# Kernel tuning notes

Hardware: AMD Instinct MI355X
Metric: run time of the kernel (lower is better)

## Reference

```python
import jax, jax.numpy as jnp
import numpy as np

NATTRS, NOBJS = 250, 400
N = NATTRS + NOBJS           # 650 graph nodes
E = 100000                   # edges
D_IN, D_HID, D_NODE = 512, 4096, 512
FEAT, EMB, B = 2048, 800, 256
LN_EPS = 1e-5


def setup_inputs() -> dict:
    key = jax.random.key(0)
    ks = jax.random.split(key, 32)
    w = lambda k, shape: (jax.random.normal(k, shape, jnp.float32) / np.sqrt(shape[-1])).astype(jnp.float32)
    return {
        'img': jax.random.normal(ks[0], (B, FEAT), jnp.float32),
        'nodes': jax.random.normal(ks[1], (N, D_IN), jnp.float32),
        'edge_src': jax.random.randint(ks[2], (E,), 0, N),
        'edge_dst': jax.random.randint(ks[3], (E,), 0, N),
        'W1l': w(ks[4], (D_HID, D_IN)), 'b1': jnp.zeros((D_HID,), jnp.float32), 'W1r': w(ks[5], (D_HID, D_IN)),
        'W2l': w(ks[6], (D_NODE, D_HID)), 'b2': jnp.zeros((D_NODE,), jnp.float32), 'W2r': w(ks[7], (D_NODE, D_HID)),
        'Wp1': w(ks[8], (1200, 2 * D_NODE)), 'bp1': jnp.zeros((1200,), jnp.float32),
        'Wp2': w(ks[9], (EMB, 1200)), 'bp2': jnp.zeros((EMB,), jnp.float32),
        'gp': jnp.ones((EMB,), jnp.float32), 'bpn': jnp.zeros((EMB,), jnp.float32),
        'Wi1': w(ks[10], (768, FEAT)), 'bi1': jnp.zeros((768,), jnp.float32),
        'Wi2': w(ks[11], (1000, 768)), 'bi2': jnp.zeros((1000,), jnp.float32),
        'Wi3': w(ks[12], (EMB, 1000)), 'bi3': jnp.zeros((EMB,), jnp.float32),
        'gi': jnp.ones((EMB,), jnp.float32), 'bin_': jnp.zeros((EMB,), jnp.float32),
    }


def _segment_mean(x, src, dst, n):
    # gather source features, mean-aggregate at destinations (PyG SAGEConv 'mean')
    agg = jax.ops.segment_sum(x[src], dst, num_segments=n)
    deg = jax.ops.segment_sum(jnp.ones_like(dst, dtype=x.dtype), dst, num_segments=n)
    return agg / jnp.clip(deg, 1.0)[:, None]


def _sage(x, src, dst, Wl, bl, Wr):
    # out_i = lin_l(mean_{j in N(i)} x_j) + lin_r(x_i); lin_r has no bias in PyG
    return _segment_mean(x, src, dst, x.shape[0]) @ Wl.T + bl + x @ Wr.T


def _ln(x, g, b):
    m = x.mean(-1, keepdims=True)
    v = ((x - m) ** 2).mean(-1, keepdims=True)
    return (x - m) / jnp.sqrt(v + LN_EPS) * g + b


def reference(img, nodes, edge_src, edge_dst, W1l, b1, W1r, W2l, b2, W2r,
              Wp1, bp1, Wp2, bp2, gp, bpn, Wi1, bi1, Wi2, bi2, Wi3, bi3, gi, bin_):
    # GCN backbone (dropout is identity in eval)
    h = jax.nn.relu(_sage(nodes, edge_src, edge_dst, W1l, b1, W1r))
    out_nodes = _sage(h, edge_src, edge_dst, W2l, b2, W2r)          # [N, 512]
    # all attr-obj pairs: attr repeated per obj, objs tiled per attr
    attr = out_nodes[:NATTRS]
    obj = out_nodes[NATTRS:]
    pa = jnp.repeat(attr, NOBJS, axis=0)                            # [P, 512]
    po = jnp.tile(obj, (NATTRS, 1))                                 # [P, 512]
    pairs = jnp.concatenate([pa, po], axis=1)                       # [P, 1024]
    # pair_fc: Linear-ReLU -> Linear -> LayerNorm
    p = jax.nn.relu(pairs @ Wp1.T + bp1)
    p = _ln(p @ Wp2.T + bp2, gp, bpn)                               # [P, 800]
    # img_fc: two hidden Linear-ReLU -> Linear -> LayerNorm
    i = jax.nn.relu(img @ Wi1.T + bi1)
    i = jax.nn.relu(i @ Wi2.T + bi2)
    i = _ln(i @ Wi3.T + bi3, gi, bin_)                              # [B, 800]
    return i @ p.T                                                  # [B, P]
```

## Files before the change

kernel.cpp:

```cpp
#include <hip/hip_runtime.h>

#define NN 650
#define NE 100000

typedef short bf16x8_t __attribute__((ext_vector_type(8)));
typedef short s16x4_t __attribute__((ext_vector_type(4)));
typedef float f32x4_t __attribute__((ext_vector_type(4)));

__device__ __forceinline__ unsigned short f2bf(float f) {
  union { float f; unsigned u; } x; x.f = f;
  unsigned r = x.u + 0x7fffu + ((x.u >> 16) & 1u);
  return (unsigned short)(r >> 16);
}
__device__ __forceinline__ float bf2f(unsigned short u) {
  union { unsigned u; float f; } x; x.u = ((unsigned)u) << 16; return x.f;
}

typedef const __attribute__((address_space(1))) unsigned int* gptr_t;
typedef __attribute__((address_space(3))) unsigned int* lptr_t;
__device__ __forceinline__ void gl_lds16(const unsigned short* g, unsigned short* l) {
  __builtin_amdgcn_global_load_lds((gptr_t)g, (lptr_t)l, 16, 0, 0);
}

__global__ void k_scatter(const int* __restrict__ src, const int* __restrict__ dst,
                          float* __restrict__ C, float* __restrict__ deg) {
  int e = blockIdx.x * 256 + threadIdx.x;
  if (e < NE) {
    int s = src[e], d = dst[e];
    atomicAdd(&C[d * NN + s], 1.0f);
    atomicAdd(&deg[d], 1.0f);
  }
}

__global__ void k_adj_norm(const float* __restrict__ C, const float* __restrict__ deg,
                           unsigned short* __restrict__ Cn) {
  int idx = blockIdx.x * 256 + threadIdx.x;
  if (idx >= 768 * 672) return;
  int i = idx / 672, j = idx - i * 672;
  float v = (i < NN && j < NN) ? C[i * NN + j] / fmaxf(deg[i], 1.0f) : 0.0f;
  Cn[idx] = f2bf(v);
}

#define MAXJ 12
struct CvtDesc { const float* src; unsigned short* dst; int Mvalid, Kin, ldi, off, ldo, nElem, nblk; };
struct CvtPack { CvtDesc d[MAXJ]; };
__global__ void k_cvt_all(CvtPack P) {
  int b = blockIdx.x;
  int j = 0;
  while (b >= P.d[j].nblk) { b -= P.d[j].nblk; ++j; }
  const CvtDesc D = P.d[j];
  int idx = b * 256 + threadIdx.x;
  if (idx >= D.nElem) return;
  int r = idx / D.ldo, c = idx - r * D.ldo;
  D.dst[idx] = (r < D.Mvalid && c < D.Kin) ? f2bf(D.src[(size_t)r * D.ldi + D.off + c]) : (unsigned short)0;
}

__global__ void k_ttr(const unsigned short* __restrict__ in, unsigned short* __restrict__ out,
                      int ldi, int ldo) {
  __shared__ unsigned short tile[64][65];
  const int c0 = blockIdx.x * 64, r0 = blockIdx.y * 64;
  const int t = threadIdx.x;
  const int rl = t >> 4, cl = (t & 15) * 4;
#pragma unroll
  for (int rr = 0; rr < 4; ++rr) {
    s16x4_t v = *(const s16x4_t*)(in + (size_t)(r0 + rl + rr * 16) * ldi + c0 + cl);
#pragma unroll
    for (int j = 0; j < 4; ++j) tile[rl + rr * 16][cl + j] = (unsigned short)v[j];
  }
  __syncthreads();
  if (r0 + cl < ldo) {
#pragma unroll
    for (int cc = 0; cc < 4; ++cc) {
      int crow = rl + cc * 16;
      unsigned short o[4] = { tile[cl + 0][crow], tile[cl + 1][crow],
                              tile[cl + 2][crow], tile[cl + 3][crow] };
      *(s16x4_t*)(out + (size_t)(c0 + crow) * ldo + r0 + cl) = *(s16x4_t*)o;
    }
  }
}

__global__ void k_pgen(const float* __restrict__ Pa, const float* __restrict__ Po,
                       unsigned short* __restrict__ P, int r0, int rows) {
  int g = blockIdx.x * 256 + threadIdx.x;
  if (g >= rows * 152) return;
  int lp = g / 152, k = (g - lp * 152) * 8;
  int p = r0 + lp;
  unsigned short t8[8];
  if (p < 100000) {
    int a = p / 400, o = p - a * 400;
    const float* pa = Pa + (size_t)a * 1216 + k;
    const float* po = Po + (size_t)o * 1216 + k;
    float4 x1 = *(const float4*)(pa);
    float4 x2 = *(const float4*)(pa + 4);
    float4 y1 = *(const float4*)(po);
    float4 y2 = *(const float4*)(po + 4);
    t8[0] = f2bf(fmaxf(x1.x + y1.x, 0.f)); t8[1] = f2bf(fmaxf(x1.y + y1.y, 0.f));
    t8[2] = f2bf(fmaxf(x1.z + y1.z, 0.f)); t8[3] = f2bf(fmaxf(x1.w + y1.w, 0.f));
    t8[4] = f2bf(fmaxf(x2.x + y2.x, 0.f)); t8[5] = f2bf(fmaxf(x2.y + y2.y, 0.f));
    t8[6] = f2bf(fmaxf(x2.z + y2.z, 0.f)); t8[7] = f2bf(fmaxf(x2.w + y2.w, 0.f));
  } else {
#pragma unroll
    for (int j = 0; j < 8; ++j) t8[j] = 0;
  }
  *(bf16x8_t*)(P + (size_t)lp * 1216 + k) = *(bf16x8_t*)t8;
}

__global__ void k_stats_fin(float* __restrict__ S, float* __restrict__ SS) {
  int i = blockIdx.x * 256 + threadIdx.x;
  if (i >= 100096) return;
  float s = S[i], ss = SS[i];
  float m = s * (1.0f / 800.0f);
  float var = ss * (1.0f / 800.0f) - m * m;
  S[i] = m;
  SS[i] = rsqrtf(fmaxf(var, 0.f) + 1e-5f);
}

__global__ void k_fin_on(const float* __restrict__ acc, const float* __restrict__ bias,
                         unsigned short* __restrict__ out) {
  int i = blockIdx.x * 256 + threadIdx.x;
  if (i >= 768 * 512) return;
  int r = i >> 9, c = i & 511;
  out[i] = f2bf(r < 650 ? acc[i] + bias[c] : 0.f);
}
__global__ void k_fin_rb(const float* __restrict__ acc, const float* __restrict__ bias,
                         unsigned short* __restrict__ out, int nElem, int cols, int Nv) {
  int i = blockIdx.x * 256 + threadIdx.x;
  if (i >= nElem) return;
  int c = i % cols;
  float v = 0.f;
  if (c < Nv) v = fmaxf(acc[i] + bias[c], 0.f);
  out[i] = f2bf(v);
}

__global__ void k_prep_i(const unsigned short* __restrict__ iB,
                         const float* __restrict__ gp, const float* __restrict__ bpn,
                         unsigned short* __restrict__ iG,
                         float* __restrict__ c1, float* __restrict__ c2) {
  const int row = blockIdx.x, t = threadIdx.x;
  float s1 = 0.f, s2 = 0.f;
  if (t < 100) {
    bf16x8_t v = *(const bf16x8_t*)(iB + (size_t)row * 800 + t * 8);
    unsigned short o[8];
#pragma unroll
    for (int j = 0; j < 8; ++j) {
      float f = bf2f((unsigned short)v[j]);
      float g = gp[t * 8 + j];
      s1 += f * g; s2 += f * bpn[t * 8 + j];
      o[j] = f2bf(f * g);
    }
    *(bf16x8_t*)(iG + (size_t)row * 800 + t * 8) = *(bf16x8_t*)o;
  }
#pragma unroll
  for (int off = 32; off > 0; off >>= 1) { s1 += __shfl_down(s1, off); s2 += __shfl_down(s2, off); }
  __shared__ float sh[4];
  int w = t >> 6, lane = t & 63;
  if (lane == 0) { sh[w] = s1; sh[2 + w] = s2; }
  __syncthreads();
  if (t == 0) { c1[row] = sh[0] + sh[1]; c2[row] = sh[2] + sh[3]; }
}

#define BK 32
template<int OUT_BF, int RELU, int LNF, int QST, int SK>
__launch_bounds__(256)
__global__ void k_gemm128(const unsigned short* __restrict__ A,
                          const unsigned short* __restrict__ B,
                          const float* __restrict__ bias,
                          const float* __restrict__ addb,
                          void* __restrict__ Cout,
                          int K, int ldc,
                          int Mvalid, int Nvalid, int Nstore, int swap, int swz,
                          const float* __restrict__ lnm, const float* __restrict__ lninv,
                          const float* __restrict__ lnc1, const float* __restrict__ lnc2,
                          float* __restrict__ sumP, float* __restrict__ ssP) {
  __shared__ unsigned short As[2][128 * BK];
  __shared__ unsigned short Bs[2][128 * BK];
  const int tid = threadIdx.x;
  const int w = tid >> 6, lane = tid & 63;
  int bx = blockIdx.x, by = blockIdx.y;
  if (swz) {
    int T = gridDim.x * gridDim.y;
    int flat = blockIdx.x + gridDim.x * blockIdx.y;
    int xcd = flat & 7, s = flat >> 3;
    int qq = T >> 3, rr = T & 7;
    int slot = (xcd < rr ? xcd * (qq + 1) : rr * (qq + 1) + (xcd - rr) * qq) + s;
    bx = slot % gridDim.x; by = slot / gridDim.x;
  }
  const int bm = swap ? by : bx;
  const int bn = swap ? bx : by;
  const int m0 = bm * 128, n0 = bn * 128;
  const int wm = w & 1, wn = w >> 1;
  const int lr = lane & 15, q = lane >> 4;

  const int srow = w * 32 + (lane >> 2);
  const int mw_ = ((lane >> 2) & 3) ^ ((lane >> 4) & 3);
  const int scol = (((lane & 3) ^ mw_) * 8);
  const int mr_ = (lane & 3) ^ ((lane >> 2) & 3);
  const int qe = ((q ^ mr_) * 8);

  int nt = K / BK, kt0 = 0;
  if (SK) { int Ksl = K / (int)gridDim.z; nt = Ksl / BK; kt0 = blockIdx.z * (Ksl / BK); }

  const unsigned short* Ag = A + (size_t)(m0 + srow) * K + (size_t)kt0 * BK + scol;
  const unsigned short* Bg = B + (size_t)(n0 + srow) * K + (size_t)kt0 * BK + scol;
  const int so0 = (w * 32) * BK;
  const int so1 = (w * 32 + 16) * BK;

  f32x4_t acc[4][4];
#pragma unroll
  for (int r = 0; r < 4; ++r)
#pragma unroll
    for (int t = 0; t < 4; ++t) { f32x4_t z = {0.f, 0.f, 0.f, 0.f}; acc[r][t] = z; }

  gl_lds16(Ag, &As[0][so0]); gl_lds16(Ag + 16 * (size_t)K, &As[0][so1]);
  gl_lds16(Bg, &Bs[0][so0]); gl_lds16(Bg + 16 * (size_t)K, &Bs[0][so1]);
  Ag += BK; Bg += BK;

  for (int t = 0; t < nt; ++t) {
    const int cur = t & 1;
    __syncthreads();
    if (t + 1 < nt) {
      const int nxt = cur ^ 1;
      gl_lds16(Ag, &As[nxt][so0]); gl_lds16(Ag + 16 * (size_t)K, &As[nxt][so1]);
      gl_lds16(Bg, &Bs[nxt][so0]); gl_lds16(Bg + 16 * (size_t)K, &Bs[nxt][so1]);
      Ag += BK; Bg += BK;
    }
    bf16x8_t af[4], bfv[4];
#pragma unroll
    for (int r = 0; r < 4; ++r)
      af[r] = *(const bf16x8_t*)(&As[cur][(wm * 64 + r * 16 + lr) * BK + qe]);
#pragma unroll
    for (int tt = 0; tt < 4; ++tt)
      bfv[tt] = *(const bf16x8_t*)(&Bs[cur][(wn * 64 + tt * 16 + lr) * BK + qe]);
#pragma unroll
    for (int r = 0; r < 4; ++r)
#pragma unroll
      for (int tt = 0; tt < 4; ++tt)
        acc[r][tt] = __builtin_amdgcn_mfma_f32_16x16x32_bf16(af[r], bfv[tt], acc[r][tt], 0, 0, 0);
  }

  if (SK) {
#pragma unroll
    for (int r = 0; r < 4; ++r)
#pragma unroll
      for (int t = 0; t < 4; ++t)
#pragma unroll
        for (int e = 0; e < 4; ++e) {
          int gm = m0 + wm * 64 + r * 16 + q * 4 + e;
          int gn = n0 + wn * 64 + t * 16 + lr;
          if (gm < Mvalid && gn < Nvalid)
            atomicAdd((float*)Cout + (size_t)gm * ldc + gn, acc[r][t][e]);
        }
  } else if (QST) {
#pragma unroll
    for (int r = 0; r < 4; ++r) {
#pragma unroll
      for (int e = 0; e < 4; ++e) {
        const int gm = m0 + wm * 64 + r * 16 + q * 4 + e;
        float s = 0.f, ss = 0.f;
#pragma unroll
        for (int t = 0; t < 4; ++t) {
          const int gn = n0 + wn * 64 + t * 16 + lr;
          float v = 0.f;
          if (gm < Mvalid && gn < Nvalid) v = acc[r][t][e] + bias[gn];
          if (gn < Nstore)
            ((unsigned short*)Cout)[(size_t)gm * ldc + gn] = f2bf(v);
          s += v; ss += v * v;
        }
#pragma unroll
        for (int m = 1; m < 16; m <<= 1) {
          s += __shfl_xor(s, m);
          ss += __shfl_xor(ss, m);
        }
        if (lr == 0 && gm < Mvalid) {
          atomicAdd(&sumP[gm], s);
          atomicAdd(&ssP[gm], ss);
        }
      }
    }
  } else {
#pragma unroll
    for (int r = 0; r < 4; ++r) {
#pragma unroll
      for (int t = 0; t < 4; ++t) {
#pragma unroll
        for (int e = 0; e < 4; ++e) {
          int gm = m0 + wm * 64 + r * 16 + q * 4 + e;
          int gn = n0 + wn * 64 + t * 16 + lr;
          if (gn < Nstore) {
            float v = 0.f;
            if (gm < Mvalid && gn < Nvalid) {
              v = acc[r][t][e];
              if (LNF) {
                v = lninv[gn] * (v - lnm[gn] * lnc1[gm]) + lnc2[gm];
              } else {
                if (bias) v += bias[gn];
                if (addb) v += addb[(size_t)gm * ldc + gn];
                if (RELU) v = fmaxf(v, 0.f);
              }
            }
            if (OUT_BF) ((unsigned short*)Cout)[(size_t)gm * ldc + gn] = f2bf(v);
            else        ((float*)Cout)[(size_t)gm * ldc + gn] = v;
          }
        }
      }
    }
  }
}

__global__ void k_ln_img(const float* __restrict__ in, const float* __restrict__ bb,
                         unsigned short* __restrict__ out,
                         const float* __restrict__ g, const float* __restrict__ b) {
  const int row = blockIdx.x, t = threadIdx.x;
  float v[4]; float s = 0.f, ss = 0.f; int j = 0;
  for (int idx = t; idx < 800; idx += 256, ++j) {
    float x = in[(size_t)row * 800 + idx] + bb[idx];
    v[j] = x; s += x; ss += x * x;
  }
#pragma unroll
  for (int off = 32; off > 0; off >>= 1) {
    s += __shfl_down(s, off);
    ss += __shfl_down(ss, off);
  }
  __shared__ float sh[8];
  int wave = t >> 6, lane = t & 63;
  if (lane == 0) { sh[wave] = s; sh[4 + wave] = ss; }
  __syncthreads();
  if (t == 0) {
    float S = sh[0] + sh[1] + sh[2] + sh[3];
    float SS = sh[4] + sh[5] + sh[6] + sh[7];
    float m = S * (1.0f / 800.0f);
    float var = SS * (1.0f / 800.0f) - m * m;
    sh[0] = m; sh[1] = rsqrtf(fmaxf(var, 0.f) + 1e-5f);
  }
  __syncthreads();
  float m = sh[0], inv = sh[1];
  j = 0;
  for (int idx = t; idx < 800; idx += 256, ++j) {
    float y = (v[j] - m) * inv * g[idx] + b[idx];
    out[(size_t)row * 800 + idx] = f2bf(y);
  }
}

extern "C" void kernel_launch(void* const* d_in, const int* in_sizes, int n_in,
                              void* d_out, int out_size, void* d_ws, size_t ws_size,
                              hipStream_t stream) {
  (void)in_sizes; (void)n_in; (void)out_size; (void)ws_size;
  const float* img  = (const float*)d_in[0];
  const float* nodes= (const float*)d_in[1];
  const int* esrc   = (const int*)d_in[2];
  const int* edst   = (const int*)d_in[3];
  const float* W1l  = (const float*)d_in[4];
  const float* b1   = (const float*)d_in[5];
  const float* W1r  = (const float*)d_in[6];
  const float* W2l  = (const float*)d_in[7];
  const float* b2   = (const float*)d_in[8];
  const float* W2r  = (const float*)d_in[9];
  const float* Wp1  = (const float*)d_in[10];
  const float* bp1  = (const float*)d_in[11];
  const float* Wp2  = (const float*)d_in[12];
  const float* bp2  = (const float*)d_in[13];
  const float* gp   = (const float*)d_in[14];
  const float* bpn  = (const float*)d_in[15];
  const float* Wi1  = (const float*)d_in[16];
  const float* bi1  = (const float*)d_in[17];
  const float* Wi2  = (const float*)d_in[18];
  const float* bi2  = (const float*)d_in[19];
  const float* Wi3  = (const float*)d_in[20];
  const float* bi3  = (const float*)d_in[21];
  const float* gi   = (const float*)d_in[22];
  const float* binp = (const float*)d_in[23];

  char* wsp = (char*)d_ws;
  auto alloc = [&](size_t bytes) -> void* {
    void* p = (void*)wsp; wsp += (bytes + 255) & ~(size_t)255; return p;
  };
  unsigned short* onB    = (unsigned short*)alloc((size_t)768 * 512 * 2);
  unsigned short* Wp1LB  = (unsigned short*)alloc((size_t)1280 * 512 * 2);
  unsigned short* Wp1RB  = (unsigned short*)alloc((size_t)1280 * 512 * 2);
  unsigned short* Wp2B   = (unsigned short*)alloc((size_t)896 * 1216 * 2);
  float* PaB             = (float*)alloc((size_t)256 * 1216 * 4);
  float* PoB             = (float*)alloc((size_t)512 * 1216 * 4);
  unsigned short* imgB   = (unsigned short*)alloc((size_t)256 * 2048 * 2);
  unsigned short* Wi1B   = (unsigned short*)alloc((size_t)768 * 2048 * 2);
  unsigned short* Wi2B   = (unsigned short*)alloc((size_t)1024 * 768 * 2);
  unsigned short* Wi3B   = (unsigned short*)alloc((size_t)896 * 1024 * 2);
  unsigned short* i1B    = (unsigned short*)alloc((size_t)256 * 768 * 2);
  unsigned short* i2B    = (unsigned short*)alloc((size_t)256 * 1024 * 2);
  float* i3F             = (float*)alloc((size_t)256 * 800 * 4);
  unsigned short* iB     = (unsigned short*)alloc((size_t)256 * 800 * 2);
  unsigned short* iG     = (unsigned short*)alloc((size_t)256 * 800 * 2);
  float* c1B             = (float*)alloc(256 * 4);
  float* c2B             = (float*)alloc(256 * 4);
  float* mArr            = (float*)alloc((size_t)100096 * 4);
  float* ivArr           = (float*)alloc((size_t)100096 * 4);
  unsigned short* qB     = (unsigned short*)alloc((size_t)100096 * 800 * 2);

  char* swp = (char*)qB;
  auto salloc = [&](size_t bytes) -> void* {
    void* p = (void*)swp; swp += (bytes + 255) & ~(size_t)255; return p;
  };
  float* adjC            = (float*)salloc((size_t)NN * NN * 4);
  float* deg             = (float*)salloc(NN * 4);
  unsigned short* Cn     = (unsigned short*)salloc((size_t)768 * 672 * 2);
  unsigned short* nodesB = (unsigned short*)salloc((size_t)768 * 512 * 2);
  unsigned short* nodesT = (unsigned short*)salloc((size_t)512 * 672 * 2);
  unsigned short* agg1   = (unsigned short*)salloc((size_t)768 * 512 * 2);
  float* tmp1            = (float*)salloc((size_t)768 * 4096 * 4);
  unsigned short* hB     = (unsigned short*)salloc((size_t)768 * 4096 * 2);
  unsigned short* hT     = (unsigned short*)salloc((size_t)4096 * 672 * 2);
  unsigned short* agg2   = (unsigned short*)salloc((size_t)768 * 4096 * 2);
  float* tmp2            = (float*)salloc((size_t)768 * 512 * 4);
  unsigned short* W1lB   = (unsigned short*)salloc((size_t)4096 * 512 * 2);
  unsigned short* W1rB   = (unsigned short*)salloc((size_t)4096 * 512 * 2);
  unsigned short* W2lB   = (unsigned short*)salloc((size_t)512 * 4096 * 2);
  unsigned short* W2rB   = (unsigned short*)salloc((size_t)512 * 4096 * 2);
  float* F1              = (float*)salloc((size_t)256 * 768 * 4);
  float* F2              = (float*)salloc((size_t)256 * 1024 * 4);

  unsigned short* Pch = (unsigned short*)d_out;

  hipMemsetAsync(adjC, 0, (size_t)NN * NN * 4, stream);
  hipMemsetAsync(deg, 0, NN * 4, stream);
  hipMemsetAsync(mArr, 0, (size_t)100096 * 4, stream);
  hipMemsetAsync(ivArr, 0, (size_t)100096 * 4, stream);
  hipMemsetAsync(tmp2, 0, (size_t)768 * 512 * 4, stream);
  hipMemsetAsync(F1, 0, (size_t)256 * 768 * 4, stream);
  hipMemsetAsync(F2, 0, (size_t)256 * 1024 * 4, stream);
  hipMemsetAsync(i3F, 0, (size_t)256 * 800 * 4, stream);

  k_scatter<<<dim3((NE + 255) / 256), 256, 0, stream>>>(esrc, edst, adjC, deg);
  k_adj_norm<<<dim3((768 * 672 + 255) / 256), 256, 0, stream>>>(adjC, deg, Cn);

  {
    CvtPack pk; int nj = 0, tot = 0;
    auto addj = [&](const float* s, unsigned short* d, int Mv, int Mp, int Kin, int ldi, int off, int ldo) {
      int ne = Mp * ldo, nb = (ne + 255) / 256;
      pk.d[nj++] = { s, d, Mv, Kin, ldi, off, ldo, ne, nb };
      tot += nb;
    };
    addj(nodes, nodesB, 650, 768, 512, 512, 0, 512);
    addj(W1l, W1lB, 4096, 4096, 512, 512, 0, 512);
    addj(W1r, W1rB, 4096, 4096, 512, 512, 0, 512);
    addj(W2l, W2lB, 512, 512, 4096, 4096, 0, 4096);
    addj(W2r, W2rB, 512, 512, 4096, 4096, 0, 4096);
    addj(Wp1, Wp1LB, 1200, 1280, 512, 1024, 0, 512);
    addj(Wp1, Wp1RB, 1200, 1280, 512, 1024, 512, 512);
    addj(Wp2, Wp2B, 800, 896, 1200, 1200, 0, 1216);
    addj(Wi1, Wi1B, 768, 768, 2048, 2048, 0, 2048);
    addj(Wi2, Wi2B, 1000, 1024, 768, 768, 0, 768);
    addj(Wi3, Wi3B, 800, 896, 1000, 1000, 0, 1024);
    addj(img, imgB, 256, 256, 2048, 2048, 0, 2048);
    k_cvt_all<<<dim3(tot), 256, 0, stream>>>(pk);
  }

  k_ttr<<<dim3(512 / 64, (672 + 63) / 64), 256, 0, stream>>>(nodesB, nodesT, 512, 672);

#define NUL nullptr, nullptr, nullptr, nullptr, nullptr, nullptr
  k_gemm128<1, 0, 0, 0, 0><<<dim3(6, 4), 256, 0, stream>>>(Cn, nodesT, nullptr, nullptr, agg1, 672, 512, 650, 512, 512, 0, 0, NUL);
  k_gemm128<0, 0, 0, 0, 0><<<dim3(6, 32), 256, 0, stream>>>(agg1, W1lB, b1, nullptr, tmp1, 512, 4096, 650, 4096, 4096, 0, 0, NUL);
  k_gemm128<1, 1, 0, 0, 0><<<dim3(6, 32), 256, 0, stream>>>(nodesB, W1rB, nullptr, tmp1, hB, 512, 4096, 650, 4096, 4096, 0, 0, NUL);
  k_ttr<<<dim3(4096 / 64, (672 + 63) / 64), 256, 0, stream>>>(hB, hT, 4096, 672);
  k_gemm128<1, 0, 0, 0, 0><<<dim3(6, 32), 256, 0, stream>>>(Cn, hT, nullptr, nullptr, agg2, 672, 4096, 650, 4096, 4096, 0, 0, NUL);
  k_gemm128<0, 0, 0, 0, 1><<<dim3(6, 4, 8), 256, 0, stream>>>(agg2, W2lB, nullptr, nullptr, tmp2, 4096, 512, 650, 512, 512, 0, 0, NUL);
  k_gemm128<0, 0, 0, 0, 1><<<dim3(6, 4, 8), 256, 0, stream>>>(hB, W2rB, nullptr, nullptr, tmp2, 4096, 512, 650, 512, 512, 0, 0, NUL);
  k_fin_on<<<dim3((768 * 512 + 255) / 256), 256, 0, stream>>>(tmp2, b2, onB);
  k_gemm128<0, 0, 0, 0, 0><<<dim3(2, 10), 256, 0, stream>>>(onB, Wp1LB, bp1, nullptr, PaB, 512, 1216, 250, 1200, 1216, 0, 0, NUL);
  k_gemm128<0, 0, 0, 0, 0><<<dim3(4, 10), 256, 0, stream>>>(onB + 250 * 512, Wp1RB, nullptr, nullptr, PoB, 512, 1216, 400, 1200, 1216, 0, 0, NUL);

  k_gemm128<0, 0, 0, 0, 1><<<dim3(2, 6, 8), 256, 0, stream>>>(imgB, Wi1B, nullptr, nullptr, F1, 2048, 768, 256, 768, 768, 0, 0, NUL);
  k_fin_rb<<<dim3((256 * 768 + 255) / 256), 256, 0, stream>>>(F1, bi1, i1B, 256 * 768, 768, 768);
  k_gemm128<0, 0, 0, 0, 1><<<dim3(2, 8, 8), 256, 0, stream>>>(i1B, Wi2B, nullptr, nullptr, F2, 768, 1024, 256, 1000, 1024, 0, 0, NUL);
  k_fin_rb<<<dim3((256 * 1024 + 255) / 256), 256, 0, stream>>>(F2, bi2, i2B, 256 * 1024, 1024, 1000);
  k_gemm128<0, 0, 0, 0, 1><<<dim3(2, 7, 8), 256, 0, stream>>>(i2B, Wi3B, nullptr, nullptr, i3F, 1024, 800, 256, 800, 800, 0, 0, NUL);
  k_ln_img<<<dim3(256), 256, 0, stream>>>(i3F, bi3, iB, gi, binp);
  k_prep_i<<<dim3(256), 128, 0, stream>>>(iB, gp, bpn, iG, c1B, c2B);

  const int CB = 262;
  for (int c = 0; c < 3; ++c) {
    int b0 = c * CB;
    int nb = (782 - b0) < CB ? (782 - b0) : CB;
    int r0 = b0 * 128;
    int rows = nb * 128;
    k_pgen<<<dim3((rows * 152 + 255) / 256), 256, 0, stream>>>(PaB, PoB, Pch, r0, rows);
    int mv = (100000 - r0) < rows ? (100000 - r0) : rows;
    k_gemm128<1, 0, 0, 1, 0><<<dim3(7, nb), 256, 0, stream>>>(Pch, Wp2B, bp2, nullptr,
        qB + (size_t)r0 * 800, 1216, 800, mv, 800, 800, 1, 1,
        nullptr, nullptr, nullptr, nullptr, mArr + r0, ivArr + r0);
  }
  k_stats_fin<<<dim3((100096 + 255) / 256), 256, 0, stream>>>(mArr, ivArr);

  k_gemm128<0, 0, 1, 0, 0><<<dim3(2, 782), 256, 0, stream>>>(iG, qB, nullptr, nullptr, (float*)d_out,
      800, 100000, 256, 100000, 100000, 0, 1, mArr, ivArr, c1B, c2B, nullptr, nullptr);
#undef NUL
}
```

Measured before the change: 1.094 ms.

## Fuse pair generation into the pair_fc second GEMM A-tile load

Removes the separate k_pgen kernel that materialized the relu(Pa[a]+Po[o]) bf16 pair matrix in chunks. The new k_qfused kernel instead builds each A tile in LDS on the fly, reading fp32 Pa/Po rows from registers prefetched one stage ahead. It also computes the bias add and the per-row sum and sum-of-squares for LayerNorm, accumulated with atomics. This avoids writing and re-reading a roughly 240MB intermediate and cuts launches, at the cost of more global fp32 reads per tile (Pa/Po are reloaded by each of the 7 N-blocks) and conversion work inside the GEMM loop.

```diff
diff --git a/kernel.cpp b/kernel.cpp
--- a/kernel.cpp
+++ b/kernel.cpp
@@ -77,32 +77,6 @@
       *(s16x4_t*)(out + (size_t)(c0 + crow) * ldo + r0 + cl) = *(s16x4_t*)o;
     }
   }
-}
-
-__global__ void k_pgen(const float* __restrict__ Pa, const float* __restrict__ Po,
-                       unsigned short* __restrict__ P, int r0, int rows) {
-  int g = blockIdx.x * 256 + threadIdx.x;
-  if (g >= rows * 152) return;
-  int lp = g / 152, k = (g - lp * 152) * 8;
-  int p = r0 + lp;
-  unsigned short t8[8];
-  if (p < 100000) {
-    int a = p / 400, o = p - a * 400;
-    const float* pa = Pa + (size_t)a * 1216 + k;
-    const float* po = Po + (size_t)o * 1216 + k;
-    float4 x1 = *(const float4*)(pa);
-    float4 x2 = *(const float4*)(pa + 4);
-    float4 y1 = *(const float4*)(po);
-    float4 y2 = *(const float4*)(po + 4);
-    t8[0] = f2bf(fmaxf(x1.x + y1.x, 0.f)); t8[1] = f2bf(fmaxf(x1.y + y1.y, 0.f));
-    t8[2] = f2bf(fmaxf(x1.z + y1.z, 0.f)); t8[3] = f2bf(fmaxf(x1.w + y1.w, 0.f));
-    t8[4] = f2bf(fmaxf(x2.x + y2.x, 0.f)); t8[5] = f2bf(fmaxf(x2.y + y2.y, 0.f));
-    t8[6] = f2bf(fmaxf(x2.z + y2.z, 0.f)); t8[7] = f2bf(fmaxf(x2.w + y2.w, 0.f));
-  } else {
-#pragma unroll
-    for (int j = 0; j < 8; ++j) t8[j] = 0;
-  }
-  *(bf16x8_t*)(P + (size_t)lp * 1216 + k) = *(bf16x8_t*)t8;
 }
 
 __global__ void k_stats_fin(float* __restrict__ S, float* __restrict__ SS) {
@@ -302,6 +276,139 @@
             else        ((float*)Cout)[(size_t)gm * ldc + gn] = v;
           }
         }
+      }
+    }
+  }
+}
+
+__device__ __forceinline__ void pack16(const float4& x1, const float4& x2,
+                                       const float4& y1, const float4& y2,
+                                       unsigned short* dst) {
+  unsigned short o8[8];
+  o8[0] = f2bf(fmaxf(x1.x + y1.x, 0.f));
+  o8[1] = f2bf(fmaxf(x1.y + y1.y, 0.f));
+  o8[2] = f2bf(fmaxf(x1.z + y1.z, 0.f));
+  o8[3] = f2bf(fmaxf(x1.w + y1.w, 0.f));
+  o8[4] = f2bf(fmaxf(x2.x + y2.x, 0.f));
+  o8[5] = f2bf(fmaxf(x2.y + y2.y, 0.f));
+  o8[6] = f2bf(fmaxf(x2.z + y2.z, 0.f));
+  o8[7] = f2bf(fmaxf(x2.w + y2.w, 0.f));
+  *(bf16x8_t*)dst = *(bf16x8_t*)o8;
+}
+
+__launch_bounds__(256)
+__global__ void k_qfused(const float* __restrict__ Pa, const float* __restrict__ Po,
+                         const unsigned short* __restrict__ B,
+                         const float* __restrict__ bias,
+                         unsigned short* __restrict__ C,
+                         float* __restrict__ sumP, float* __restrict__ ssP) {
+  __shared__ unsigned short As[2][128 * 32];
+  __shared__ unsigned short Bs[2][128 * 32];
+  const int tid = threadIdx.x;
+  const int w = tid >> 6, lane = tid & 63;
+  {
+  }
+  const int T = gridDim.x * gridDim.y;
+  const int flat = blockIdx.x + gridDim.x * blockIdx.y;
+  const int xcd = flat & 7, sI = flat >> 3;
+  const int qq = T >> 3, rr = T & 7;
+  const int slot = (xcd < rr ? xcd * (qq + 1) : rr * (qq + 1) + (xcd - rr) * qq) + sI;
+  const int bm = slot % gridDim.x, bn = slot / gridDim.x;
+  const int m0 = bm * 128, n0 = bn * 128;
+  const int wm = w & 1, wn = w >> 1;
+  const int lr = lane & 15, q = lane >> 4;
+  const int srow = w * 32 + (lane >> 2);
+  const int scol = (lane & 3) * 8;
+
+  const int p0 = m0 + srow, p1 = p0 + 16;
+  const int a0 = p0 / 400, o0 = p0 - a0 * 400;
+  const int a1 = p1 / 400, o1 = p1 - a1 * 400;
+  const float* pa0 = Pa + (size_t)a0 * 1216 + scol;
+  const float* po0 = Po + (size_t)o0 * 1216 + scol;
+  const float* pa1 = Pa + (size_t)a1 * 1216 + scol;
+  const float* po1 = Po + (size_t)o1 * 1216 + scol;
+
+  const unsigned short* Bg = B + (size_t)(n0 + srow) * 1216 + scol;
+  const int so0 = (w * 32) * 32;
+  const int so1 = (w * 32 + 16) * 32;
+  const int aw0 = srow * 32 + scol;
+  const int aw1 = (srow + 16) * 32 + scol;
+
+  f32x4_t acc[4][4];
+#pragma unroll
+  for (int r = 0; r < 4; ++r)
+#pragma unroll
+    for (int t = 0; t < 4; ++t) { f32x4_t z = {0.f, 0.f, 0.f, 0.f}; acc[r][t] = z; }
+
+  const int nt = 38;
+
+  gl_lds16(Bg, &Bs[0][so0]); gl_lds16(Bg + 16 * 1216, &Bs[0][so1]); Bg += 32;
+  float4 xa, xb, ya, yb, za, zb, wa, wb;
+  xa = *(const float4*)(pa0);     xb = *(const float4*)(pa0 + 4);
+  ya = *(const float4*)(po0);     yb = *(const float4*)(po0 + 4);
+  za = *(const float4*)(pa1);     zb = *(const float4*)(pa1 + 4);
+  wa = *(const float4*)(po1);     wb = *(const float4*)(po1 + 4);
+  pack16(xa, xb, ya, yb, &As[0][aw0]);
+  pack16(za, zb, wa, wb, &As[0][aw1]);
+  xa = *(const float4*)(pa0 + 32); xb = *(const float4*)(pa0 + 36);
+  ya = *(const float4*)(po0 + 32); yb = *(const float4*)(po0 + 36);
+  za = *(const float4*)(pa1 + 32); zb = *(const float4*)(pa1 + 36);
+  wa = *(const float4*)(po1 + 32); wb = *(const float4*)(po1 + 36);
+
+  for (int t = 0; t < nt; ++t) {
+    const int cur = t & 1, nxt = cur ^ 1;
+    __syncthreads();
+    if (t + 1 < nt) {
+      gl_lds16(Bg, &Bs[nxt][so0]); gl_lds16(Bg + 16 * 1216, &Bs[nxt][so1]); Bg += 32;
+    }
+    bf16x8_t af[4], bfv[4];
+#pragma unroll
+    for (int r = 0; r < 4; ++r)
+      af[r] = *(const bf16x8_t*)(&As[cur][(wm * 64 + r * 16 + lr) * 32 + q * 8]);
+#pragma unroll
+    for (int tt = 0; tt < 4; ++tt)
+      bfv[tt] = *(const bf16x8_t*)(&Bs[cur][(wn * 64 + tt * 16 + lr) * 32 + q * 8]);
+#pragma unroll
+    for (int r = 0; r < 4; ++r)
+#pragma unroll
+      for (int tt = 0; tt < 4; ++tt)
+        acc[r][tt] = __builtin_amdgcn_mfma_f32_16x16x32_bf16(af[r], bfv[tt], acc[r][tt], 0, 0, 0);
+    if (t + 1 < nt) {
+      pack16(xa, xb, ya, yb, &As[nxt][aw0]);
+      pack16(za, zb, wa, wb, &As[nxt][aw1]);
+      if (t + 2 < nt) {
+        const int kn = (t + 2) * 32;
+        xa = *(const float4*)(pa0 + kn); xb = *(const float4*)(pa0 + kn + 4);
+        ya = *(const float4*)(po0 + kn); yb = *(const float4*)(po0 + kn + 4);
+        za = *(const float4*)(pa1 + kn); zb = *(const float4*)(pa1 + kn + 4);
+        wa = *(const float4*)(po1 + kn); wb = *(const float4*)(po1 + kn + 4);
+      }
+    }
+  }
+
+#pragma unroll
+  for (int r = 0; r < 4; ++r) {
+#pragma unroll
+    for (int e = 0; e < 4; ++e) {
+      const int gm = m0 + wm * 64 + r * 16 + q * 4 + e;
+      float s = 0.f, ss = 0.f;
+#pragma unroll
+      for (int t = 0; t < 4; ++t) {
+        const int gn = n0 + wn * 64 + t * 16 + lr;
+        float v = 0.f;
+        if (gm < 100000 && gn < 800) v = acc[r][t][e] + bias[gn];
+        if (gn < 800)
+          C[(size_t)gm * 800 + gn] = f2bf(v);
+        s += v; ss += v * v;
+      }
+#pragma unroll
+      for (int m = 1; m < 16; m <<= 1) {
+        s += __shfl_xor(s, m);
+        ss += __shfl_xor(ss, m);
+      }
+      if (lr == 0 && gm < 100000) {
+        atomicAdd(&sumP[gm], s);
+        atomicAdd(&ssP[gm], ss);
       }
     }
   }
@@ -417,8 +524,6 @@
   float* F1              = (float*)salloc((size_t)256 * 768 * 4);
   float* F2              = (float*)salloc((size_t)256 * 1024 * 4);
 
-  unsigned short* Pch = (unsigned short*)d_out;
-
   hipMemsetAsync(adjC, 0, (size_t)NN * NN * 4, stream);
   hipMemsetAsync(deg, 0, NN * 4, stream);
   hipMemsetAsync(mArr, 0, (size_t)100096 * 4, stream);
@@ -475,18 +580,7 @@
   k_ln_img<<<dim3(256), 256, 0, stream>>>(i3F, bi3, iB, gi, binp);
   k_prep_i<<<dim3(256), 128, 0, stream>>>(iB, gp, bpn, iG, c1B, c2B);
 
-  const int CB = 262;
-  for (int c = 0; c < 3; ++c) {
-    int b0 = c * CB;
-    int nb = (782 - b0) < CB ? (782 - b0) : CB;
-    int r0 = b0 * 128;
-    int rows = nb * 128;
-    k_pgen<<<dim3((rows * 152 + 255) / 256), 256, 0, stream>>>(PaB, PoB, Pch, r0, rows);
-    int mv = (100000 - r0) < rows ? (100000 - r0) : rows;
-    k_gemm128<1, 0, 0, 1, 0><<<dim3(7, nb), 256, 0, stream>>>(Pch, Wp2B, bp2, nullptr,
-        qB + (size_t)r0 * 800, 1216, 800, mv, 800, 800, 1, 1,
-        nullptr, nullptr, nullptr, nullptr, mArr + r0, ivArr + r0);
-  }
+  k_qfused<<<dim3(782, 7), 256, 0, stream>>>(PaB, PoB, Wp2B, bp2, qB, mArr, ivArr);
   k_stats_fin<<<dim3((100096 + 255) / 256), 256, 0, stream>>>(mArr, ivArr);
 
   k_gemm128<0, 0, 1, 0, 0><<<dim3(2, 782), 256, 0, stream>>>(iG, qB, nullptr, nullptr, (float*)d_out,
```

Result: slower. 1.197 ms (+9.5%).

## Add 256x128-tile GEMM kernel for pair projection and final similarity

Applied to the files above, without the earlier changes.

Introduces a new GEMM kernel with a 256-row by 128-column block tile, giving each wave a 128x64 sub-tile so more MFMA work is done per LDS load. It replaces the 128x128 kernel in the two largest GEMMs: the pair-embedding projection with fused row statistics, and the final image-by-pair product with the fused LayerNorm correction. Chunking is rescaled to 256-row blocks. The larger accumulator array raises register pressure and may lower occupancy. For the final product the whole 256-row image batch now fits in one tile, so each qB tile is read once instead of twice.

```diff
diff --git a/kernel.cpp b/kernel.cpp
--- a/kernel.cpp
+++ b/kernel.cpp
@@ -300,6 +300,140 @@
             }
             if (OUT_BF) ((unsigned short*)Cout)[(size_t)gm * ldc + gn] = f2bf(v);
             else        ((float*)Cout)[(size_t)gm * ldc + gn] = v;
+          }
+        }
+      }
+    }
+  }
+}
+
+template<int LNF, int QST>
+__launch_bounds__(256)
+__global__ void k_gemm256(const unsigned short* __restrict__ A,
+                          const unsigned short* __restrict__ B,
+                          const float* __restrict__ bias,
+                          void* __restrict__ Cout,
+                          int K, int ldc,
+                          int Mvalid, int Nvalid, int Nstore, int swap,
+                          const float* __restrict__ lnm, const float* __restrict__ lninv,
+                          const float* __restrict__ lnc1, const float* __restrict__ lnc2,
+                          float* __restrict__ sumP, float* __restrict__ ssP) {
+  __shared__ unsigned short As[2][256 * 32];
+  __shared__ unsigned short Bs[2][128 * 32];
+  const int tid = threadIdx.x;
+  const int w = tid >> 6, lane = tid & 63;
+  int bx = blockIdx.x, by = blockIdx.y;
+  {
+    int T = gridDim.x * gridDim.y;
+    int flat = blockIdx.x + gridDim.x * blockIdx.y;
+    int xcd = flat & 7, sI = flat >> 3;
+    int qq = T >> 3, rr = T & 7;
+    int slot = (xcd < rr ? xcd * (qq + 1) : rr * (qq + 1) + (xcd - rr) * qq) + sI;
+    bx = slot % gridDim.x; by = slot / gridDim.x;
+  }
+  const int bm = swap ? by : bx;
+  const int bn = swap ? bx : by;
+  const int m0 = bm * 256, n0 = bn * 128;
+  const int wm = w & 1, wn = w >> 1;
+  const int lr = lane & 15, q = lane >> 4;
+
+  const int mw_ = ((lane >> 2) & 3) ^ ((lane >> 4) & 3);
+  const int scol = (((lane & 3) ^ mw_) * 8);
+  const int mr_ = (lane & 3) ^ ((lane >> 2) & 3);
+  const int qe = ((q ^ mr_) * 8);
+
+  const unsigned short* Ag = A + (size_t)(m0 + w * 16 + (lane >> 2)) * K + scol;
+  const unsigned short* Bg = B + (size_t)(n0 + w * 16 + (lane >> 2)) * K + scol;
+  const int sa = (w * 16) * 32;
+  const int sb = (w * 16) * 32;
+
+  f32x4_t acc[8][4];
+#pragma unroll
+  for (int r = 0; r < 8; ++r)
+#pragma unroll
+    for (int t = 0; t < 4; ++t) { f32x4_t z = {0.f, 0.f, 0.f, 0.f}; acc[r][t] = z; }
+
+  const int nt = K / 32;
+
+  gl_lds16(Ag,                     &As[0][sa]);
+  gl_lds16(Ag + (size_t)64 * K,    &As[0][sa + 64 * 32]);
+  gl_lds16(Ag + (size_t)128 * K,   &As[0][sa + 128 * 32]);
+  gl_lds16(Ag + (size_t)192 * K,   &As[0][sa + 192 * 32]);
+  gl_lds16(Bg,                     &Bs[0][sb]);
+  gl_lds16(Bg + (size_t)64 * K,    &Bs[0][sb + 64 * 32]);
+  Ag += 32; Bg += 32;
+
+  for (int t = 0; t < nt; ++t) {
+    const int cur = t & 1;
+    __syncthreads();
+    if (t + 1 < nt) {
+      const int nxt = cur ^ 1;
+      gl_lds16(Ag,                   &As[nxt][sa]);
+      gl_lds16(Ag + (size_t)64 * K,  &As[nxt][sa + 64 * 32]);
+      gl_lds16(Ag + (size_t)128 * K, &As[nxt][sa + 128 * 32]);
+      gl_lds16(Ag + (size_t)192 * K, &As[nxt][sa + 192 * 32]);
+      gl_lds16(Bg,                   &Bs[nxt][sb]);
+      gl_lds16(Bg + (size_t)64 * K,  &Bs[nxt][sb + 64 * 32]);
+      Ag += 32; Bg += 32;
+    }
+    bf16x8_t af[8], bfv[4];
+#pragma unroll
+    for (int r = 0; r < 8; ++r)
+      af[r] = *(const bf16x8_t*)(&As[cur][(wm * 128 + r * 16 + lr) * 32 + qe]);
+#pragma unroll
+    for (int tt = 0; tt < 4; ++tt)
+      bfv[tt] = *(const bf16x8_t*)(&Bs[cur][(wn * 64 + tt * 16 + lr) * 32 + qe]);
+#pragma unroll
+    for (int r = 0; r < 8; ++r)
+#pragma unroll
+      for (int tt = 0; tt < 4; ++tt)
+        acc[r][tt] = __builtin_amdgcn_mfma_f32_16x16x32_bf16(af[r], bfv[tt], acc[r][tt], 0, 0, 0);
+  }
+
+  if (QST) {
+#pragma unroll
+    for (int r = 0; r < 8; ++r) {
+#pragma unroll
+      for (int e = 0; e < 4; ++e) {
+        const int gm = m0 + wm * 128 + r * 16 + q * 4 + e;
+        float s = 0.f, ss = 0.f;
+#pragma unroll
+        for (int t = 0; t < 4; ++t) {
+          const int gn = n0 + wn * 64 + t * 16 + lr;
+          float v = 0.f;
+          if (gm < Mvalid && gn < Nvalid) v = acc[r][t][e] + bias[gn];
+          if (gn < Nstore)
+            ((unsigned short*)Cout)[(size_t)gm * ldc + gn] = f2bf(v);
+          s += v; ss += v * v;
+        }
+#pragma unroll
+        for (int m = 1; m < 16; m <<= 1) {
+          s += __shfl_xor(s, m);
+          ss += __shfl_xor(ss, m);
+        }
+        if (lr == 0 && gm < Mvalid) {
+          atomicAdd(&sumP[gm], s);
+          atomicAdd(&ssP[gm], ss);
+        }
+      }
+    }
+  } else {
+#pragma unroll
+    for (int r = 0; r < 8; ++r) {
+#pragma unroll
+      for (int t = 0; t < 4; ++t) {
+#pragma unroll
+        for (int e = 0; e < 4; ++e) {
+          int gm = m0 + wm * 128 + r * 16 + q * 4 + e;
+          int gn = n0 + wn * 64 + t * 16 + lr;
+          if (gn < Nstore) {
+            float v = 0.f;
+            if (gm < Mvalid && gn < Nvalid) {
+              v = acc[r][t][e];
+              if (LNF) v = lninv[gn] * (v - lnm[gn] * lnc1[gm]) + lnc2[gm];
+              else if (bias) v += bias[gn];
+            }
+            ((float*)Cout)[(size_t)gm * ldc + gn] = v;
           }
         }
       }
@@ -475,21 +609,22 @@
   k_ln_img<<<dim3(256), 256, 0, stream>>>(i3F, bi3, iB, gi, binp);
   k_prep_i<<<dim3(256), 128, 0, stream>>>(iB, gp, bpn, iG, c1B, c2B);
 
-  const int CB = 262;
+  const int CBm = 131;
+  const int NBtot = 391;
   for (int c = 0; c < 3; ++c) {
-    int b0 = c * CB;
-    int nb = (782 - b0) < CB ? (782 - b0) : CB;
-    int r0 = b0 * 128;
-    int rows = nb * 128;
+    int b0 = c * CBm;
+    int nb = (NBtot - b0) < CBm ? (NBtot - b0) : CBm;
+    int r0 = b0 * 256;
+    int rows = nb * 256;
     k_pgen<<<dim3((rows * 152 + 255) / 256), 256, 0, stream>>>(PaB, PoB, Pch, r0, rows);
     int mv = (100000 - r0) < rows ? (100000 - r0) : rows;
-    k_gemm128<1, 0, 0, 1, 0><<<dim3(7, nb), 256, 0, stream>>>(Pch, Wp2B, bp2, nullptr,
-        qB + (size_t)r0 * 800, 1216, 800, mv, 800, 800, 1, 1,
+    k_gemm256<0, 1><<<dim3(7, nb), 256, 0, stream>>>(Pch, Wp2B, bp2,
+        qB + (size_t)r0 * 800, 1216, 800, mv, 800, 800, 1,
         nullptr, nullptr, nullptr, nullptr, mArr + r0, ivArr + r0);
   }
   k_stats_fin<<<dim3((100096 + 255) / 256), 256, 0, stream>>>(mArr, ivArr);
 
-  k_gemm128<0, 0, 1, 0, 0><<<dim3(2, 782), 256, 0, stream>>>(iG, qB, nullptr, nullptr, (float*)d_out,
-      800, 100000, 256, 100000, 100000, 0, 1, mArr, ivArr, c1B, c2B, nullptr, nullptr);
+  k_gemm256<1, 0><<<dim3(782, 1), 256, 0, stream>>>(iG, qB, nullptr, (float*)d_out,
+      800, 100000, 256, 100000, 100000, 1, mArr, ivArr, c1B, c2B, nullptr, nullptr);
 #undef NUL
 }
```

After: 1.544 ms. 41.2% more time.
